# Performance work log

Measured on AMD Instinct MI355X. Metric: run time of the kernel, lower is better.

Reference implementation:

```python
import jax, jax.numpy as jnp
import numpy as np

DEGREES = [1, 2, 3]
SEG_IDS = np.repeat(np.arange(len(DEGREES)), [2 * l + 1 for l in DEGREES])  # (m_tot,)
M_TOT = int(SEG_IDS.shape[0])  # 15
N_NODES, F, F_IN, N_TYPE = 24576, 512, 512, 10


def setup_inputs() -> dict:
    key = jax.random.key(0)
    ks = jax.random.split(key, 8)
    s = 1.0 / np.sqrt(F).astype(np.float32)
    return {
        "x": jax.random.normal(ks[0], (N_NODES, F_IN), jnp.float32),
        "chi": jax.random.normal(ks[1], (N_NODES, M_TOT), jnp.float32),
        "z_one_hot": jax.nn.one_hot(jax.random.randint(ks[2], (N_NODES,), 0, N_TYPE), N_TYPE, dtype=jnp.float32),
        "W1": jax.random.normal(ks[3], (F_IN, F), jnp.float32) * s,
        "b1": jnp.zeros((F,), jnp.float32),
        "W2": jax.random.normal(ks[4], (F, F), jnp.float32) * s,
        "W3": jax.random.normal(ks[5], (F, 1), jnp.float32) * s,
        "W4": jax.random.normal(ks[6], (len(DEGREES) * F, F_IN), jnp.float32) * (1.0 / np.sqrt(len(DEGREES) * F).astype(np.float32)),
        "b4": jnp.zeros((F_IN,), jnp.float32),
    }


def _l0_contraction(x_chi):
    # make_l0_contraction_fn(degrees), vmapped over the feature axis:
    # per degree l, sum over its (2l+1) m-components of x_chi**2.
    # x_chi: (n, m_tot, F) -> (n, n_degrees, F)
    sq = jnp.swapaxes(x_chi * x_chi, 0, 1)  # (m_tot, n, F)
    out = jax.ops.segment_sum(sq, jnp.asarray(SEG_IDS), num_segments=len(DEGREES))
    return jnp.swapaxes(out, 0, 1)


def reference(x, chi, z_one_hot, W1, b1, W2, W3, W4, b4):
    # max_body_order == 2 -> SymmetricContraction branch is skipped (x_chi_bo = x_chi)
    h = x @ W1 + b1                              # Dense(features)(x): (n, F)
    x_chi = h[:, None, :] * chi[:, :, None]      # (n, m_tot, F)
    x_chi = x_chi @ W2                           # Dense(features, use_bias=False): (n, m_tot, F)
    chi_bo = (x_chi @ W3)[..., 0]                # Dense(1, use_bias=False).squeeze(-1): (n, m_tot)
    inv = _l0_contraction(x_chi).reshape(x.shape[0], -1)  # (n, n_degrees*F)
    x_bo = jax.nn.silu(inv @ W4 + b4)            # Dense(x.shape[-1]): (n, F_in)
    return (x_bo, chi_bo)
```

## Files before the change

kernel.cpp:

```cpp
#include <hip/hip_runtime.h>

typedef __bf16 bf16_t;
typedef __bf16 bf16x8 __attribute__((ext_vector_type(8)));
typedef float f32x4 __attribute__((ext_vector_type(4)));

#define BK 64


__device__ __forceinline__ void g2l16(const void* g, void* l) {
    __builtin_amdgcn_global_load_lds((__attribute__((address_space(1))) void*)(g),
                                     (__attribute__((address_space(3))) void*)(l),
                                     16, 0, 0);
}

#define SB()  __builtin_amdgcn_sched_barrier(0)
#define BAR() __builtin_amdgcn_s_barrier()

__global__ __launch_bounds__(1024)
void gemm16_kernel(const bf16_t* __restrict__ A, const bf16_t* __restrict__ Bt,
                   const float* __restrict__ bias, void* __restrict__ Cout,
                   int N, int K, int mode)
{
    __shared__ __align__(16) bf16_t lA[2][12288];
    __shared__ __align__(16) bf16_t lB[2][16384];

    const int tid  = threadIdx.x;
    const int lane = tid & 63;
    const int wave = tid >> 6;
    const int wr   = wave >> 2;
    const int wc   = wave & 3;
    const int l15  = lane & 15;
    const int lh   = lane >> 4;

    const int bm = blockIdx.x;
    const int bn = blockIdx.y;

    const size_t strb = (size_t)K * 2;

    const int q0 = tid * 16;
    const size_t ro = (size_t)(q0 >> 7) * strb + ((q0 ^ (((q0 >> 7) & 7) << 4)) & 127);
    const char* gA = (const char*)A  + (size_t)bm * 192 * strb + ro;
    const char* gB = (const char*)Bt + (size_t)bn * 256 * strb + ro;
    char* baseA = (char*)&lA[0][0];
    char* baseB = (char*)&lB[0][0];

    auto stage = [&](int t, int buf) {
        const size_t kb = (size_t)t * 128;
        g2l16(gA + kb, baseA + buf * 24576 + q0);
        if (tid < 512)
            g2l16(gA + kb + 128 * strb, baseA + buf * 24576 + 16384 + q0);
        g2l16(gB + kb, baseB + buf * 32768 + q0);
        g2l16(gB + kb + 128 * strb, baseB + buf * 32768 + 16384 + q0);
    };

    const int swzr = (l15 & 7) << 4;
    const int xk0  = (lh * 16) ^ swzr;
    const int xk1  = (64 + lh * 16) ^ swzr;
    const int aOff = (wr * 48 + l15) * 128;
    const int bOff = (wc * 64 + l15) * 128;

    f32x4 acc[3][4] = {};

    const int T = K / BK;
    stage(0, 0);

    for (int t = 0; t < T; ++t) {
        const int buf = t & 1;

        asm volatile("s_waitcnt vmcnt(0)" ::: "memory");
        BAR();
        SB();

        if (t + 1 < T) stage(t + 1, buf ^ 1);
        SB();

        bf16x8 af[3][2], bf[4][2];
        {
            const char* _pa = baseA + buf * 24576 + aOff;
#pragma unroll
            for (int m = 0; m < 3; ++m) {
                af[m][0] = *(const bf16x8*)(_pa + m * 2048 + xk0);
                af[m][1] = *(const bf16x8*)(_pa + m * 2048 + xk1);
            }
            const char* _pb = baseB + buf * 32768 + bOff;
#pragma unroll
            for (int n = 0; n < 4; ++n) {
                bf[n][0] = *(const bf16x8*)(_pb + n * 2048 + xk0);
                bf[n][1] = *(const bf16x8*)(_pb + n * 2048 + xk1);
            }
        }

        __builtin_amdgcn_s_setprio(1);
#pragma unroll
        for (int m = 0; m < 3; ++m)
#pragma unroll
        for (int n = 0; n < 4; ++n)
#pragma unroll
        for (int kk = 0; kk < 2; ++kk)
            acc[m][n] = __builtin_amdgcn_mfma_f32_16x16x32_bf16(
                af[m][kk], bf[n][kk], acc[m][n], 0, 0, 0);
        __builtin_amdgcn_s_setprio(0);
    }

    const int gr0 = bm * 192 + wr * 48 + lh * 4;
    const int gc0 = bn * 256 + wc * 64 + l15;
    if (mode == 0) {
        bf16_t* C = (bf16_t*)Cout;
#pragma unroll
        for (int m = 0; m < 3; ++m)
#pragma unroll
        for (int n = 0; n < 4; ++n) {
            const int c = gc0 + n * 16;
            const float bv = bias ? bias[c] : 0.f;
#pragma unroll
            for (int j = 0; j < 4; ++j) {
                const int r = gr0 + m * 16 + j;
                C[(size_t)r * N + c] = (bf16_t)(acc[m][n][j] + bv);
            }
        }
    } else {
        float* C = (float*)Cout;
#pragma unroll
        for (int m = 0; m < 3; ++m)
#pragma unroll
        for (int n = 0; n < 4; ++n) {
            const int c = gc0 + n * 16;
            const float bv = bias[c];
#pragma unroll
            for (int j = 0; j < 4; ++j) {
                const int r = gr0 + m * 16 + j;
                float v = acc[m][n][j] + bv;
                C[(size_t)r * N + c] = v / (1.f + __expf(-v));
            }
        }
    }
}

template<int MF>
__global__ __launch_bounds__(512)
void gemm_bt_kernel(const bf16_t* __restrict__ A, const bf16_t* __restrict__ Bt,
                    const float* __restrict__ bias, void* __restrict__ Cout,
                    int N, int K, int mode)
{
    constexpr int MF2    = MF / 2;
    constexpr int NFA    = MF;
    constexpr int ABYTES = MF * 4096;
    constexpr int RA     = MF / 2;

    __shared__ __align__(16) bf16_t lA[2][MF * 2048];
    __shared__ __align__(16) bf16_t lB[2][16384];

    const int tid  = threadIdx.x;
    const int lane = tid & 63;
    const int wave = tid >> 6;
    const int wr   = wave >> 2;
    const int wc   = wave & 3;
    const int l15  = lane & 15;
    const int lh   = lane >> 4;

    const int bm = blockIdx.x;
    const int bn = blockIdx.y;

    const size_t strb = (size_t)K * 2;

    const int q0 = tid * 16;
    const size_t rowOff = (size_t)(q0 >> 7) * strb + ((q0 ^ (((q0 >> 7) & 7) << 4)) & 127);
    const char* gA = (const char*)A  + (size_t)bm * (MF * 32) * strb + rowOff;
    const char* gB = (const char*)Bt + (size_t)bn * 256 * strb + rowOff;
    char* baseA = (char*)&lA[0][0];
    char* baseB = (char*)&lB[0][0];

    auto stageA = [&](int t, int buf, int r) {
        g2l16(gA + (size_t)t * 128 + (size_t)(r * 64) * strb,
              baseA + buf * ABYTES + r * 8192 + q0);
    };
    auto stageB = [&](int t, int buf, int r) {
        g2l16(gB + (size_t)t * 128 + (size_t)(r * 64) * strb,
              baseB + buf * 32768 + r * 8192 + q0);
    };

    const int swzr = (l15 & 7) << 4;
    const int xk0  = (lh * 16) ^ swzr;
    const int xk1  = (64 + lh * 16) ^ swzr;
    const int aOff = wr * (MF2 * 2) * 2048 + l15 * 128;
    const int bOff = wc * 8192 + l15 * 128;

    f32x4 acc[2][2][MF2][2] = {};

    const int T = K / BK;

#pragma unroll
    for (int r = 0; r < RA; ++r) stageA(0, 0, r);
#pragma unroll
    for (int r = 0; r < 4; ++r)  stageB(0, 0, r);

    for (int t = 0; t < T; ++t) {
        const int buf = t & 1, nbuf = buf ^ 1;

        asm volatile("s_waitcnt vmcnt(0)" ::: "memory");
        BAR();
        SB();

        if (t + 1 < T) {
#pragma unroll
            for (int r = 0; r < RA; ++r) stageA(t + 1, nbuf, r);
#pragma unroll
            for (int r = 0; r < 4; ++r)  stageB(t + 1, nbuf, r);
        }
        SB();

        bf16x8 af[NFA][2], bf[4][2];
        {
            const char* _pa = baseA + buf * ABYTES + aOff;
#pragma unroll
            for (int i = 0; i < NFA; ++i) {
                af[i][0] = *(const bf16x8*)(_pa + i * 2048 + xk0);
                af[i][1] = *(const bf16x8*)(_pa + i * 2048 + xk1);
            }
            const char* _pb = baseB + buf * 32768 + bOff;
#pragma unroll
            for (int j = 0; j < 4; ++j) {
                bf[j][0] = *(const bf16x8*)(_pb + j * 2048 + xk0);
                bf[j][1] = *(const bf16x8*)(_pb + j * 2048 + xk1);
            }
        }

        __builtin_amdgcn_s_setprio(1);
#pragma unroll
        for (int mh = 0; mh < 2; ++mh)
#pragma unroll
        for (int nh = 0; nh < 2; ++nh)
#pragma unroll
        for (int m = 0; m < MF2; ++m)
#pragma unroll
        for (int n = 0; n < 2; ++n)
#pragma unroll
        for (int kk = 0; kk < 2; ++kk)
            acc[mh][nh][m][n] = __builtin_amdgcn_mfma_f32_16x16x32_bf16(
                af[mh * MF2 + m][kk], bf[nh * 2 + n][kk], acc[mh][nh][m][n], 0, 0, 0);
        __builtin_amdgcn_s_setprio(0);
    }

    const int gr0 = bm * (MF * 32) + wr * (MF2 * 32) + lh * 4;
    const int gc0 = bn * 256 + wc * 64 + l15;
    if (mode == 0) {
        bf16_t* C = (bf16_t*)Cout;
#pragma unroll
        for (int mh = 0; mh < 2; ++mh)
#pragma unroll
        for (int nh = 0; nh < 2; ++nh)
#pragma unroll
        for (int m = 0; m < MF2; ++m)
#pragma unroll
        for (int n = 0; n < 2; ++n) {
            const int c = gc0 + nh * 32 + n * 16;
            const float bv = bias ? bias[c] : 0.f;
#pragma unroll
            for (int j = 0; j < 4; ++j) {
                const int r = gr0 + (mh * MF2 + m) * 16 + j;
                C[(size_t)r * N + c] = (bf16_t)(acc[mh][nh][m][n][j] + bv);
            }
        }
    } else {
        float* C = (float*)Cout;
#pragma unroll
        for (int mh = 0; mh < 2; ++mh)
#pragma unroll
        for (int nh = 0; nh < 2; ++nh)
#pragma unroll
        for (int m = 0; m < MF2; ++m)
#pragma unroll
        for (int n = 0; n < 2; ++n) {
            const int c = gc0 + nh * 32 + n * 16;
            const float bv = bias[c];
#pragma unroll
            for (int j = 0; j < 4; ++j) {
                const int r = gr0 + (mh * MF2 + m) * 16 + j;
                float v = acc[mh][nh][m][n][j] + bv;
                C[(size_t)r * N + c] = v / (1.f + __expf(-v));
            }
        }
    }
}

__global__ void cast8_kernel(const float* __restrict__ in, bf16_t* __restrict__ out, int n8) {
    const int i = blockIdx.x * blockDim.x + threadIdx.x;
    if (i >= n8) return;
    const float4* p = (const float4*)in + (size_t)i * 2;
    float4 a = p[0], b = p[1];
    bf16x8 v;
    v[0] = (bf16_t)a.x; v[1] = (bf16_t)a.y; v[2] = (bf16_t)a.z; v[3] = (bf16_t)a.w;
    v[4] = (bf16_t)b.x; v[5] = (bf16_t)b.y; v[6] = (bf16_t)b.z; v[7] = (bf16_t)b.w;
    *(bf16x8*)(out + (size_t)i * 8) = v;
}

__global__ void prep_kernel(const float* __restrict__ W1, bf16_t* __restrict__ W1b,
                            const float* __restrict__ W2, bf16_t* __restrict__ W2t,
                            const float* __restrict__ W4, bf16_t* __restrict__ W4t)
{
    const int b = blockIdx.x;
    if (b < 128) {
        const int i = b * 256 + threadIdx.x;
        const float4* p = (const float4*)W1 + (size_t)i * 2;
        float4 a = p[0], c = p[1];
        bf16x8 v;
        v[0] = (bf16_t)a.x; v[1] = (bf16_t)a.y; v[2] = (bf16_t)a.z; v[3] = (bf16_t)a.w;
        v[4] = (bf16_t)c.x; v[5] = (bf16_t)c.y; v[6] = (bf16_t)c.z; v[7] = (bf16_t)c.w;
        *(bf16x8*)(W1b + (size_t)i * 8) = v;
    } else if (b < 1152) {
        const int idx = (b - 128) * 256 + threadIdx.x;
        const int c = idx >> 9, r = idx & 511;
        W2t[idx] = (bf16_t)W2[(size_t)r * 512 + c];
    } else {
        const int idx = (b - 1152) * 256 + threadIdx.x;
        const int c = idx / 1536, r = idx - c * 1536;
        W4t[idx] = (bf16_t)W4[(size_t)r * 512 + c];
    }
}

__global__ void vecmat_kernel(const float* __restrict__ v, const float* __restrict__ W,
                              float* __restrict__ out) {
    const int t = blockIdx.x * blockDim.x + threadIdx.x;
    if (t >= 512) return;
    float s = 0.f;
    for (int i = 0; i < 512; ++i) s += v[i] * W[i * 512 + t];
    out[t] = s;
}

__global__ __launch_bounds__(256)
void mid_kernel(const bf16_t* __restrict__ G, const float* __restrict__ chi,
                const float* __restrict__ W3, float* __restrict__ chbo,
                bf16_t* __restrict__ A3)
{
    const int node = blockIdx.x * 4 + (threadIdx.x >> 6);
    const int lane = threadIdx.x & 63;

    const bf16x8 gv = *(const bf16x8*)(G + (size_t)node * 512 + lane * 8);
    float g[8];
#pragma unroll
    for (int j = 0; j < 8; ++j) g[j] = (float)gv[j];

    float s = 0.f;
    const float* w = W3 + lane * 8;
#pragma unroll
    for (int j = 0; j < 8; ++j) s += g[j] * w[j];
#pragma unroll
    for (int off = 32; off > 0; off >>= 1) s += __shfl_xor(s, off, 64);

    const float* ch = chi + (size_t)node * 15;
    float c0 = 0.f, c1 = 0.f, c2 = 0.f;
#pragma unroll
    for (int m = 0; m < 3; ++m)  c0 += ch[m] * ch[m];
#pragma unroll
    for (int m = 3; m < 8; ++m)  c1 += ch[m] * ch[m];
#pragma unroll
    for (int m = 8; m < 15; ++m) c2 += ch[m] * ch[m];

    if (lane < 15) chbo[(size_t)node * 15 + lane] = ch[lane] * s;

    const float cl[3] = {c0, c1, c2};
    bf16_t* arow = A3 + (size_t)node * 1536 + lane * 8;
#pragma unroll
    for (int l = 0; l < 3; ++l) {
        bf16x8 o;
#pragma unroll
        for (int j = 0; j < 8; ++j) o[j] = (bf16_t)(cl[l] * g[j] * g[j]);
        *(bf16x8*)(arow + l * 512) = o;
    }
}

extern "C" void kernel_launch(void* const* d_in, const int* in_sizes, int n_in,
                              void* d_out, int out_size, void* d_ws, size_t ws_size,
                              hipStream_t stream)
{
    const float* x   = (const float*)d_in[0];
    const float* chi = (const float*)d_in[1];
    const float* W1  = (const float*)d_in[3];
    const float* b1  = (const float*)d_in[4];
    const float* W2  = (const float*)d_in[5];
    const float* W3  = (const float*)d_in[6];
    const float* W4  = (const float*)d_in[7];
    const float* b4  = (const float*)d_in[8];

    char* ws = (char*)d_ws;
    bf16_t* W1b = (bf16_t*)(ws + 0);
    bf16_t* W2t = (bf16_t*)(ws + 524288);
    bf16_t* W4t = (bf16_t*)(ws + 1048576);
    bf16_t* Wct = (bf16_t*)(ws + 2621440);
    float*  bc  = (float*) (ws + 3145728);
    float*  u   = (float*) (ws + 3147776);
    bf16_t* Xb  = (bf16_t*)(ws + 3149824);
    bf16_t* A3  = (bf16_t*)(ws + 3149824);

    float*  xbo  = (float*)d_out;
    float*  chbo = (float*)d_out + (size_t)24576 * 512;
    bf16_t* Gb   = (bf16_t*)d_out;

    cast8_kernel<<<6144, 256, 0, stream>>>(x, Xb, 1572864);
    prep_kernel<<<4224, 256, 0, stream>>>(W1, W1b, W2, W2t, W4, W4t);
    vecmat_kernel<<<2, 256, 0, stream>>>(b1, W1, u);
    vecmat_kernel<<<2, 256, 0, stream>>>(u, W2, bc);

    gemm_bt_kernel<8><<<dim3(2, 2), 512, 0, stream>>>(W2t, W1b, nullptr, Wct, 512, 512, 0);

    gemm16_kernel<<<dim3(128, 2), 1024, 0, stream>>>(Xb, Wct, bc, Gb, 512, 512, 0);

    mid_kernel<<<6144, 256, 0, stream>>>(Gb, chi, W3, chbo, A3);

    gemm16_kernel<<<dim3(128, 2), 1024, 0, stream>>>(A3, W4t, b4, xbo, 512, 1536, 1);
}
```

Before: 173.5 us.

## Fuse mid-stage contraction into first GEMM epilogue and split-K the weight product

Removes the separate mid_kernel by computing the W3 projection, the squared l0 contraction and the A3 writes in the epilogue of the first big GEMM. The W3 dot product is reduced across column tiles with shuffles and atomicAdd into a scratch buffer, and a small chbo kernel then scales chi. The 512x512 weight-combine GEMM is split over K into 4 slices with a reduction kernel, raising parallelism from 4 blocks to 16. The aim is to avoid the round trip of G through memory. The cost is extra launches (a memset, c3, reduce and chbo kernels), atomics, and scattered 2-byte A3 stores in the epilogue.

Measured after the change: 164.3 us. 1.06x faster.

```diff
diff --git a/kernel.cpp b/kernel.cpp
--- a/kernel.cpp
+++ b/kernel.cpp
@@ -5,6 +5,7 @@
 typedef float f32x4 __attribute__((ext_vector_type(4)));
 
 #define BK 64
+#define NNODES 24576
 
 
 __device__ __forceinline__ void g2l16(const void* g, void* l) {
@@ -19,7 +20,9 @@
 __global__ __launch_bounds__(1024)
 void gemm16_kernel(const bf16_t* __restrict__ A, const bf16_t* __restrict__ Bt,
                    const float* __restrict__ bias, void* __restrict__ Cout,
-                   int N, int K, int mode)
+                   int N, int K, int mode,
+                   const float* __restrict__ W3, const float* __restrict__ c3v,
+                   float* __restrict__ sbuf)
 {
     __shared__ __align__(16) bf16_t lA[2][12288];
     __shared__ __align__(16) bf16_t lB[2][16384];
@@ -113,12 +116,10 @@
             const int c = gc0 + n * 16;
             const float bv = bias ? bias[c] : 0.f;
 #pragma unroll
-            for (int j = 0; j < 4; ++j) {
-                const int r = gr0 + m * 16 + j;
-                C[(size_t)r * N + c] = (bf16_t)(acc[m][n][j] + bv);
-            }
-        }
-    } else {
+            for (int j = 0; j < 4; ++j)
+                C[(size_t)(gr0 + m * 16 + j) * N + c] = (bf16_t)(acc[m][n][j] + bv);
+        }
+    } else if (mode == 1) {
         float* C = (float*)Cout;
 #pragma unroll
         for (int m = 0; m < 3; ++m)
@@ -128,26 +129,50 @@
             const float bv = bias[c];
 #pragma unroll
             for (int j = 0; j < 4; ++j) {
-                const int r = gr0 + m * 16 + j;
                 float v = acc[m][n][j] + bv;
-                C[(size_t)r * N + c] = v / (1.f + __expf(-v));
+                C[(size_t)(gr0 + m * 16 + j) * N + c] = v / (1.f + __expf(-v));
+            }
+        }
+    } else {
+        bf16_t* A3 = (bf16_t*)Cout;
+        float w3v[4], bv[4];
+#pragma unroll
+        for (int n = 0; n < 4; ++n) {
+            w3v[n] = W3[gc0 + n * 16];
+            bv[n]  = bias[gc0 + n * 16];
+        }
+#pragma unroll
+        for (int m = 0; m < 3; ++m)
+#pragma unroll
+        for (int j = 0; j < 4; ++j) {
+            const int r = gr0 + m * 16 + j;
+            float g[4], p = 0.f;
+#pragma unroll
+            for (int n = 0; n < 4; ++n) {
+                g[n] = acc[m][n][j] + bv[n];
+                p += g[n] * w3v[n];
+            }
+            p += __shfl_xor(p, 1); p += __shfl_xor(p, 2);
+            p += __shfl_xor(p, 4); p += __shfl_xor(p, 8);
+            if (l15 == 0) atomicAdd(&sbuf[r], p);
+            const float c0 = c3v[r], c1 = c3v[r + NNODES], c2 = c3v[r + 2 * NNODES];
+            bf16_t* arow = A3 + (size_t)r * 1536 + gc0;
+#pragma unroll
+            for (int n = 0; n < 4; ++n) {
+                const float g2 = g[n] * g[n];
+                arow[n * 16]        = (bf16_t)(c0 * g2);
+                arow[n * 16 + 512]  = (bf16_t)(c1 * g2);
+                arow[n * 16 + 1024] = (bf16_t)(c2 * g2);
             }
         }
     }
 }
 
-template<int MF>
 __global__ __launch_bounds__(512)
-void gemm_bt_kernel(const bf16_t* __restrict__ A, const bf16_t* __restrict__ Bt,
-                    const float* __restrict__ bias, void* __restrict__ Cout,
-                    int N, int K, int mode)
+void gemm8_kernel(const bf16_t* __restrict__ A, const bf16_t* __restrict__ Bt,
+                  void* __restrict__ Cout, int N, int K, int LD)
 {
-    constexpr int MF2    = MF / 2;
-    constexpr int NFA    = MF;
-    constexpr int ABYTES = MF * 4096;
-    constexpr int RA     = MF / 2;
-
-    __shared__ __align__(16) bf16_t lA[2][MF * 2048];
+    __shared__ __align__(16) bf16_t lA[2][16384];
     __shared__ __align__(16) bf16_t lB[2][16384];
 
     const int tid  = threadIdx.x;
@@ -160,19 +185,21 @@
 
     const int bm = blockIdx.x;
     const int bn = blockIdx.y;
-
-    const size_t strb = (size_t)K * 2;
+    const int bz = blockIdx.z;
+
+    const size_t strb = (size_t)LD * 2;
+    const size_t zoff = (size_t)bz * K * 2;
 
     const int q0 = tid * 16;
     const size_t rowOff = (size_t)(q0 >> 7) * strb + ((q0 ^ (((q0 >> 7) & 7) << 4)) & 127);
-    const char* gA = (const char*)A  + (size_t)bm * (MF * 32) * strb + rowOff;
-    const char* gB = (const char*)Bt + (size_t)bn * 256 * strb + rowOff;
+    const char* gA = (const char*)A  + (size_t)bm * 256 * strb + zoff + rowOff;
+    const char* gB = (const char*)Bt + (size_t)bn * 256 * strb + zoff + rowOff;
     char* baseA = (char*)&lA[0][0];
     char* baseB = (char*)&lB[0][0];
 
     auto stageA = [&](int t, int buf, int r) {
         g2l16(gA + (size_t)t * 128 + (size_t)(r * 64) * strb,
-              baseA + buf * ABYTES + r * 8192 + q0);
+              baseA + buf * 32768 + r * 8192 + q0);
     };
     auto stageB = [&](int t, int buf, int r) {
         g2l16(gB + (size_t)t * 128 + (size_t)(r * 64) * strb,
@@ -182,17 +209,15 @@
     const int swzr = (l15 & 7) << 4;
     const int xk0  = (lh * 16) ^ swzr;
     const int xk1  = (64 + lh * 16) ^ swzr;
-    const int aOff = wr * (MF2 * 2) * 2048 + l15 * 128;
+    const int aOff = wr * 16384 + l15 * 128;
     const int bOff = wc * 8192 + l15 * 128;
 
-    f32x4 acc[2][2][MF2][2] = {};
+    f32x4 acc[2][2][4][2] = {};
 
     const int T = K / BK;
 
 #pragma unroll
-    for (int r = 0; r < RA; ++r) stageA(0, 0, r);
-#pragma unroll
-    for (int r = 0; r < 4; ++r)  stageB(0, 0, r);
+    for (int r = 0; r < 4; ++r) { stageA(0, 0, r); stageB(0, 0, r); }
 
     for (int t = 0; t < T; ++t) {
         const int buf = t & 1, nbuf = buf ^ 1;
@@ -203,17 +228,15 @@
 
         if (t + 1 < T) {
 #pragma unroll
-            for (int r = 0; r < RA; ++r) stageA(t + 1, nbuf, r);
-#pragma unroll
-            for (int r = 0; r < 4; ++r)  stageB(t + 1, nbuf, r);
+            for (int r = 0; r < 4; ++r) { stageA(t + 1, nbuf, r); stageB(t + 1, nbuf, r); }
         }
         SB();
 
-        bf16x8 af[NFA][2], bf[4][2];
+        bf16x8 af[8][2], bf[4][2];
         {
-            const char* _pa = baseA + buf * ABYTES + aOff;
-#pragma unroll
-            for (int i = 0; i < NFA; ++i) {
+            const char* _pa = baseA + buf * 32768 + aOff;
+#pragma unroll
+            for (int i = 0; i < 8; ++i) {
                 af[i][0] = *(const bf16x8*)(_pa + i * 2048 + xk0);
                 af[i][1] = *(const bf16x8*)(_pa + i * 2048 + xk1);
             }
@@ -231,63 +254,44 @@
 #pragma unroll
         for (int nh = 0; nh < 2; ++nh)
 #pragma unroll
-        for (int m = 0; m < MF2; ++m)
+        for (int m = 0; m < 4; ++m)
 #pragma unroll
         for (int n = 0; n < 2; ++n)
 #pragma unroll
         for (int kk = 0; kk < 2; ++kk)
             acc[mh][nh][m][n] = __builtin_amdgcn_mfma_f32_16x16x32_bf16(
-                af[mh * MF2 + m][kk], bf[nh * 2 + n][kk], acc[mh][nh][m][n], 0, 0, 0);
+                af[mh * 4 + m][kk], bf[nh * 2 + n][kk], acc[mh][nh][m][n], 0, 0, 0);
         __builtin_amdgcn_s_setprio(0);
     }
 
-    const int gr0 = bm * (MF * 32) + wr * (MF2 * 32) + lh * 4;
+    float* C = (float*)Cout + (size_t)bz * 512 * 512;
+    const int gr0 = bm * 256 + wr * 128 + lh * 4;
     const int gc0 = bn * 256 + wc * 64 + l15;
-    if (mode == 0) {
-        bf16_t* C = (bf16_t*)Cout;
-#pragma unroll
-        for (int mh = 0; mh < 2; ++mh)
-#pragma unroll
-        for (int nh = 0; nh < 2; ++nh)
-#pragma unroll
-        for (int m = 0; m < MF2; ++m)
-#pragma unroll
-        for (int n = 0; n < 2; ++n) {
-            const int c = gc0 + nh * 32 + n * 16;
-            const float bv = bias ? bias[c] : 0.f;
-#pragma unroll
-            for (int j = 0; j < 4; ++j) {
-                const int r = gr0 + (mh * MF2 + m) * 16 + j;
-                C[(size_t)r * N + c] = (bf16_t)(acc[mh][nh][m][n][j] + bv);
-            }
-        }
-    } else {
-        float* C = (float*)Cout;
-#pragma unroll
-        for (int mh = 0; mh < 2; ++mh)
-#pragma unroll
-        for (int nh = 0; nh < 2; ++nh)
-#pragma unroll
-        for (int m = 0; m < MF2; ++m)
-#pragma unroll
-        for (int n = 0; n < 2; ++n) {
-            const int c = gc0 + nh * 32 + n * 16;
-            const float bv = bias[c];
-#pragma unroll
-            for (int j = 0; j < 4; ++j) {
-                const int r = gr0 + (mh * MF2 + m) * 16 + j;
-                float v = acc[mh][nh][m][n][j] + bv;
-                C[(size_t)r * N + c] = v / (1.f + __expf(-v));
-            }
-        }
+#pragma unroll
+    for (int mh = 0; mh < 2; ++mh)
+#pragma unroll
+    for (int nh = 0; nh < 2; ++nh)
+#pragma unroll
+    for (int m = 0; m < 4; ++m)
+#pragma unroll
+    for (int n = 0; n < 2; ++n) {
+        const int c = gc0 + nh * 32 + n * 16;
+#pragma unroll
+        for (int j = 0; j < 4; ++j)
+            C[(size_t)(gr0 + (mh * 4 + m) * 16 + j) * N + c] = acc[mh][nh][m][n][j];
     }
+}
+
+__global__ void wct_reduce_kernel(const float* __restrict__ p, bf16_t* __restrict__ out) {
+    const int i = blockIdx.x * 256 + threadIdx.x;
+    out[i] = (bf16_t)(p[i] + p[i + 262144] + p[i + 524288] + p[i + 786432]);
 }
 
 __global__ void cast8_kernel(const float* __restrict__ in, bf16_t* __restrict__ out, int n8) {
     const int i = blockIdx.x * blockDim.x + threadIdx.x;
     if (i >= n8) return;
-    const float4* p = (const float4*)in + (size_t)i * 2;
-    float4 a = p[0], b = p[1];
+    const float4* pp = (const float4*)in + (size_t)i * 2;
+    float4 a = pp[0], b = pp[1];
     bf16x8 v;
     v[0] = (bf16_t)a.x; v[1] = (bf16_t)a.y; v[2] = (bf16_t)a.z; v[3] = (bf16_t)a.w;
     v[4] = (bf16_t)b.x; v[5] = (bf16_t)b.y; v[6] = (bf16_t)b.z; v[7] = (bf16_t)b.w;
@@ -327,46 +331,25 @@
     out[t] = s;
 }
 
-__global__ __launch_bounds__(256)
-void mid_kernel(const bf16_t* __restrict__ G, const float* __restrict__ chi,
-                const float* __restrict__ W3, float* __restrict__ chbo,
-                bf16_t* __restrict__ A3)
-{
-    const int node = blockIdx.x * 4 + (threadIdx.x >> 6);
-    const int lane = threadIdx.x & 63;
-
-    const bf16x8 gv = *(const bf16x8*)(G + (size_t)node * 512 + lane * 8);
-    float g[8];
-#pragma unroll
-    for (int j = 0; j < 8; ++j) g[j] = (float)gv[j];
-
-    float s = 0.f;
-    const float* w = W3 + lane * 8;
-#pragma unroll
-    for (int j = 0; j < 8; ++j) s += g[j] * w[j];
-#pragma unroll
-    for (int off = 32; off > 0; off >>= 1) s += __shfl_xor(s, off, 64);
-
-    const float* ch = chi + (size_t)node * 15;
-    float c0 = 0.f, c1 = 0.f, c2 = 0.f;
-#pragma unroll
-    for (int m = 0; m < 3; ++m)  c0 += ch[m] * ch[m];
-#pragma unroll
-    for (int m = 3; m < 8; ++m)  c1 += ch[m] * ch[m];
-#pragma unroll
-    for (int m = 8; m < 15; ++m) c2 += ch[m] * ch[m];
-
-    if (lane < 15) chbo[(size_t)node * 15 + lane] = ch[lane] * s;
-
-    const float cl[3] = {c0, c1, c2};
-    bf16_t* arow = A3 + (size_t)node * 1536 + lane * 8;
-#pragma unroll
-    for (int l = 0; l < 3; ++l) {
-        bf16x8 o;
-#pragma unroll
-        for (int j = 0; j < 8; ++j) o[j] = (bf16_t)(cl[l] * g[j] * g[j]);
-        *(bf16x8*)(arow + l * 512) = o;
-    }
+__global__ void c3_kernel(const float* __restrict__ chi, float* __restrict__ c3) {
+    const int n = blockIdx.x * 256 + threadIdx.x;
+    if (n >= NNODES) return;
+    const float* ch = chi + (size_t)n * 15;
+    float a = 0.f, b = 0.f, c = 0.f;
+#pragma unroll
+    for (int m = 0; m < 3; ++m)  a += ch[m] * ch[m];
+#pragma unroll
+    for (int m = 3; m < 8; ++m)  b += ch[m] * ch[m];
+#pragma unroll
+    for (int m = 8; m < 15; ++m) c += ch[m] * ch[m];
+    c3[n] = a; c3[n + NNODES] = b; c3[n + 2 * NNODES] = c;
+}
+
+__global__ void chbo_kernel(const float* __restrict__ chi, const float* __restrict__ s,
+                            float* __restrict__ chbo) {
+    const int idx = blockIdx.x * 256 + threadIdx.x;
+    if (idx >= NNODES * 15) return;
+    chbo[idx] = chi[idx] * s[idx / 15];
 }
 
 extern "C" void kernel_launch(void* const* d_in, const int* in_sizes, int n_in,
@@ -383,29 +366,37 @@
     const float* b4  = (const float*)d_in[8];
 
     char* ws = (char*)d_ws;
-    bf16_t* W1b = (bf16_t*)(ws + 0);
-    bf16_t* W2t = (bf16_t*)(ws + 524288);
-    bf16_t* W4t = (bf16_t*)(ws + 1048576);
-    bf16_t* Wct = (bf16_t*)(ws + 2621440);
-    float*  bc  = (float*) (ws + 3145728);
-    float*  u   = (float*) (ws + 3147776);
-    bf16_t* Xb  = (bf16_t*)(ws + 3149824);
-    bf16_t* A3  = (bf16_t*)(ws + 3149824);
+    bf16_t* W1b  = (bf16_t*)(ws + 0);
+    bf16_t* W2t  = (bf16_t*)(ws + 524288);
+    bf16_t* W4t  = (bf16_t*)(ws + 1048576);
+    bf16_t* Wct  = (bf16_t*)(ws + 2621440);
+    float*  bc   = (float*) (ws + 3145728);
+    float*  u    = (float*) (ws + 3147776);
+    bf16_t* A3   = (bf16_t*)(ws + 3149824);
+    float*  Wctp = (float*) (ws + 3149824);
 
     float*  xbo  = (float*)d_out;
-    float*  chbo = (float*)d_out + (size_t)24576 * 512;
-    bf16_t* Gb   = (bf16_t*)d_out;
+    float*  chbo = (float*)d_out + (size_t)NNODES * 512;
+    char*   c0s  = (char*)d_out;
+    bf16_t* Xb   = (bf16_t*)(c0s + 0);
+    float*  c3   = (float*) (c0s + 25165824);
+    float*  sbuf = (float*) (c0s + 25460736);
 
     cast8_kernel<<<6144, 256, 0, stream>>>(x, Xb, 1572864);
     prep_kernel<<<4224, 256, 0, stream>>>(W1, W1b, W2, W2t, W4, W4t);
     vecmat_kernel<<<2, 256, 0, stream>>>(b1, W1, u);
     vecmat_kernel<<<2, 256, 0, stream>>>(u, W2, bc);
-
-    gemm_bt_kernel<8><<<dim3(2, 2), 512, 0, stream>>>(W2t, W1b, nullptr, Wct, 512, 512, 0);
-
-    gemm16_kernel<<<dim3(128, 2), 1024, 0, stream>>>(Xb, Wct, bc, Gb, 512, 512, 0);
-
-    mid_kernel<<<6144, 256, 0, stream>>>(Gb, chi, W3, chbo, A3);
-
-    gemm16_kernel<<<dim3(128, 2), 1024, 0, stream>>>(A3, W4t, b4, xbo, 512, 1536, 1);
-}
+    c3_kernel<<<96, 256, 0, stream>>>(chi, c3);
+    hipMemsetAsync(sbuf, 0, NNODES * sizeof(float), stream);
+
+    gemm8_kernel<<<dim3(2, 2, 4), 512, 0, stream>>>(W2t, W1b, Wctp, 512, 128, 512);
+    wct_reduce_kernel<<<1024, 256, 0, stream>>>(Wctp, Wct);
+
+    gemm16_kernel<<<dim3(128, 2), 1024, 0, stream>>>(
+        Xb, Wct, bc, A3, 512, 512, 3, W3, c3, sbuf);
+
+    chbo_kernel<<<1440, 256, 0, stream>>>(chi, sbuf, chbo);
+
+    gemm16_kernel<<<dim3(128, 2), 1024, 0, stream>>>(
+        A3, W4t, b4, xbo, 512, 1536, 1, nullptr, nullptr, nullptr);
+}
```
